# Optimization experiments

Measured on AMD Instinct MI355X. Metric: run time of the kernel, lower is better.

Reference implementation:

```python
import jax, jax.numpy as jnp
import numpy as np
from jax import lax

NUM_CLASSES = 21
MAX_OUT = 5          # max_output_size in tf.image.non_max_suppression
IOU_THR = 0.5        # NMS_IOU_THRESHOLD
CONF_THR = 0.5       # CONFIDENCE_THRESHOLD
NEG = -1e9           # stand-in for -inf score (suppressed / background)


def setup_inputs() -> dict:
    key = jax.random.key(0)
    k1, k2, k3 = jax.random.split(key, 3)
    B, N, C = 128, 8732, NUM_CLASSES
    logits = jax.random.normal(k1, (B, N, 4 + C), dtype=jnp.float32)
    # default boxes in corner format [ymin, xmin, ymax, xmax], valid geometry
    ctr = jax.random.uniform(k2, (N, 2), dtype=jnp.float32)                 # cy, cx
    sz = jax.random.uniform(k3, (N, 2), dtype=jnp.float32, minval=0.05, maxval=0.3)  # h, w
    default_boxes = jnp.clip(
        jnp.concatenate([ctr - sz / 2, ctr + sz / 2], axis=-1), 0.0, 1.0)
    return {"logits": logits, "default_boxes": default_boxes}


def _decode(loc, db):
    # db: [N,4] corners -> center/size (matches get_offset's tf.stack)
    cy = (db[:, 2] + db[:, 0]) / 2
    cx = (db[:, 3] + db[:, 1]) / 2
    h = db[:, 2] - db[:, 0]
    w = db[:, 3] - db[:, 1]
    # loc: [B,N,4] = (dy, dx, dh, dw)
    ncy = loc[..., 0] * h + cy
    ncx = loc[..., 1] * w + cx
    nh = jnp.exp(loc[..., 2]) * h
    nw = jnp.exp(loc[..., 3]) * w
    boxes = jnp.stack(
        [ncy - nh / 2, ncx - nw / 2, ncy + nh / 2, ncx + nw / 2], axis=-1)
    return jnp.clip(boxes, 0.0, 1.0)


def _iou_one_vs_all(box, boxes):
    # box [4], boxes [N,4], corner format
    tl = jnp.maximum(box[:2], boxes[:, :2])
    br = jnp.minimum(box[2:], boxes[:, 2:])
    wh = jnp.maximum(br - tl, 0.0)
    inter = wh[:, 0] * wh[:, 1]
    a1 = (box[2] - box[0]) * (box[3] - box[1])
    a2 = (boxes[:, 2] - boxes[:, 0]) * (boxes[:, 3] - boxes[:, 1])
    return inter / (a1 + a2 - inter + 1e-12)


def _nms_single(boxes, scores, classes_f):
    # boxes [N,4], scores [N] (background already set to NEG), classes_f [N] float
    def step(s, _):
        i = jnp.argmax(s)
        sc = s[i]
        b = boxes[i]
        valid = sc > CONF_THR  # score_threshold in tf NMS
        iou = _iou_one_vs_all(b, boxes)
        s = jnp.where(iou > IOU_THR, NEG, s)  # suppresses i too (IoU=1)
        return s, (b, classes_f[i], sc, valid)

    _, (bs, cs, ss, vs) = lax.scan(step, scores, None, length=MAX_OUT)
    # pad invalid slots with zeros (TF returns variable-length; we use fixed 5 + zero pad)
    bs = jnp.where(vs[:, None], bs, 0.0)
    cs = jnp.where(vs, cs, 0.0)
    ss = jnp.where(vs, ss, 0.0)
    return bs, cs[:, None], ss[:, None]  # [5,4], [5,1], [5,1]


def reference(logits, default_boxes):
    boxes = _decode(logits[..., :4], default_boxes)          # [B,N,4]
    probs = jax.nn.softmax(logits[..., 4:], axis=-1)         # [B,N,C]
    scores = jnp.max(probs, axis=-1)                          # [B,N]
    classes = jnp.argmax(probs, axis=-1)                      # [B,N] int
    # boolean_mask(classes != 0) expressed as score = -inf for background
    scores_eff = jnp.where(classes != 0, scores, NEG)
    det_b, det_c, det_s = jax.vmap(_nms_single)(
        boxes, scores_eff, classes.astype(jnp.float32))
    # pack detection_boxes / detection_classes / detection_scores -> [B,5,6]
    return jnp.concatenate([det_b, det_c, det_s], axis=-1)
```

## Files before the change

### kernel.cpp

```cpp
#include <hip/hip_runtime.h>

#define NEG (-1e9f)
constexpr int NCLS   = 21;
constexpr int NBOX   = 8732;
constexpr int MAXOUT = 5;
constexpr int CAP    = NBOX;
constexpr float IOU_THR  = 0.5f;
constexpr float CONF_THR = 0.5f;

__device__ __forceinline__ void process_box(
        const float* __restrict__ v,
        int idx,
        const float4* __restrict__ dbox4,
        float4* __restrict__ cand,
        int* __restrict__ cnt) {
    const int n = idx % NBOX;
    const int b = idx / NBOX;

    float4 db = dbox4[n];
    float cy = (db.z + db.x) * 0.5f;
    float cx = (db.w + db.y) * 0.5f;
    float h  = db.z - db.x;
    float w  = db.w - db.y;
    float ncy = v[0] * h + cy;
    float ncx = v[1] * w + cx;
    float nh  = expf(v[2]) * h;
    float nw  = expf(v[3]) * w;
    float y1 = fminf(fmaxf(ncy - nh * 0.5f, 0.f), 1.f);
    float x1 = fminf(fmaxf(ncx - nw * 0.5f, 0.f), 1.f);
    float y2 = fminf(fmaxf(ncy + nh * 0.5f, 0.f), 1.f);
    float x2 = fminf(fmaxf(ncx + nw * 0.5f, 0.f), 1.f);

    float m = v[4];
    int am = 0;
#pragma unroll
    for (int j = 1; j < NCLS; j++) {
        float x = v[4 + j];
        if (x > m) { m = x; am = j; }
    }
    float sum = 0.f;
#pragma unroll
    for (int j = 0; j < NCLS; j++) sum += expf(v[4 + j] - m);
    float score = 1.0f / sum;

    if (am != 0 && score > CONF_THR) {
        int p = atomicAdd(&cnt[b], 1);
        if (p < CAP) {
            float4* c = cand + ((long long)b * CAP + p) * 2;
            c[0] = make_float4(y1, x1, y2, x2);
            c[1] = make_float4(score, (float)am, (float)n, 0.f);
        }
    }
}

__global__ __launch_bounds__(128) void decode_kernel(
        const float* __restrict__ logits,
        const float4* __restrict__ dbox4,
        float4* __restrict__ cand,
        int* __restrict__ cnt,
        int BN) {
    const int g = (blockIdx.x * 128 + threadIdx.x) * 4;
    if (g >= BN) return;

    if (g + 3 < BN) {
        const float4* f4 = (const float4*)(logits + (long long)g * 25);
        float v[100];
#pragma unroll
        for (int k = 0; k < 25; k++) {
            float4 r = f4[k];
            v[4 * k + 0] = r.x; v[4 * k + 1] = r.y;
            v[4 * k + 2] = r.z; v[4 * k + 3] = r.w;
        }
#pragma unroll
        for (int j = 0; j < 4; j++)
            process_box(v + 25 * j, g + j, dbox4, cand, cnt);
    } else {
        for (int j = 0; j < 4 && g + j < BN; j++) {
            const float* L = logits + (long long)(g + j) * 25;
            float v[25];
#pragma unroll
            for (int k = 0; k < 25; k++) v[k] = L[k];
            process_box(v, g + j, dbox4, cand, cnt);
        }
    }
}

__global__ __launch_bounds__(64) void nms_kernel(
        const float4* __restrict__ cand,
        const int* __restrict__ cnt,
        float* __restrict__ out) {
    const int b    = blockIdx.x;
    const int lane = threadIdx.x;
    __shared__ float s_sc[CAP];
    __shared__ float s_id[CAP];

    const int M = min(cnt[b], CAP);
    const float4* cb = cand + (long long)b * CAP * 2;
    float* o = out + (long long)b * MAXOUT * 6;

    for (int i = lane; i < M; i += 64) {
        float4 mrec = cb[i * 2 + 1];
        s_sc[i] = mrec.x;
        s_id[i] = mrec.z;
    }

    int k = 0;
    for (; k < MAXOUT; k++) {
        float bv = -INFINITY, boid = 3.0e38f;
        int bi = -1;
        for (int i = lane; i < M; i += 64) {
            float v = s_sc[i], oid = s_id[i];
            if (v > bv || (v == bv && oid < boid)) { bv = v; boid = oid; bi = i; }
        }
        for (int mm = 32; mm >= 1; mm >>= 1) {
            float v2 = __shfl_xor(bv,   mm, 64);
            float o2 = __shfl_xor(boid, mm, 64);
            int   i2 = __shfl_xor(bi,   mm, 64);
            if (v2 > bv || (v2 == bv && o2 < boid)) { bv = v2; boid = o2; bi = i2; }
        }
        if (bi < 0 || !(bv > CONF_THR)) break;

        float4 sb = cb[bi * 2];
        if (lane == 0) {
            float4 mm2 = cb[bi * 2 + 1];
            o[k * 6 + 0] = sb.x; o[k * 6 + 1] = sb.y;
            o[k * 6 + 2] = sb.z; o[k * 6 + 3] = sb.w;
            o[k * 6 + 4] = mm2.y; o[k * 6 + 5] = bv;
        }

        float a1 = (sb.z - sb.x) * (sb.w - sb.y);
        for (int i = lane; i < M; i += 64) {
            float4 c = cb[i * 2];
            float tly = fmaxf(sb.x, c.x);
            float tlx = fmaxf(sb.y, c.y);
            float bry = fminf(sb.z, c.z);
            float brx = fminf(sb.w, c.w);
            float wh0 = fmaxf(bry - tly, 0.f);
            float wh1 = fmaxf(brx - tlx, 0.f);
            float inter = wh0 * wh1;
            float a2 = (c.z - c.x) * (c.w - c.y);
            float iou = inter / (a1 + a2 - inter + 1e-12f);
            if (iou > IOU_THR) s_sc[i] = NEG;
        }
    }
    for (int j = k * 6 + lane; j < MAXOUT * 6; j += 64) o[j] = 0.f;
}

extern "C" void kernel_launch(void* const* d_in, const int* in_sizes, int n_in,
                              void* d_out, int out_size, void* d_ws, size_t ws_size,
                              hipStream_t stream) {
    const float* logits = (const float*)d_in[0];
    const float4* dbox4 = (const float4*)d_in[1];
    float* out          = (float*)d_out;

    const int N  = in_sizes[1] / 4;
    const int B  = in_sizes[0] / (N * 25);
    const int BN = B * N;

    int* cnt = (int*)d_ws;
    float4* cand = (float4*)((char*)d_ws + (((size_t)B * sizeof(int) + 15) & ~(size_t)15));

    hipMemsetAsync(cnt, 0, (size_t)B * sizeof(int), stream);
    const int nthreads = (BN + 3) / 4;
    decode_kernel<<<(nthreads + 127) / 128, 128, 0, stream>>>(logits, dbox4, cand, cnt, BN);
    nms_kernel<<<B, 64, 0, stream>>>(cand, cnt, out);
}
```

Before: 190.2 us.

## Fuse decode and NMS into one kernel using a last-block-done counter

Merges the decode and NMS kernels into a single launch. Blocks are now grouped per batch image, and each block increments a per-batch done counter. The last finishing block for an image then runs the NMS for that image. This removes a kernel launch and lets NMS for early images overlap decode for others, but every block now reserves about 70KB of LDS for NMS scores, which may sharply limit occupancy during the bandwidth-bound decode phase.

Measured after the change: 374.1 us. +96.7%, slower.

```diff
diff --git a/kernel.cpp b/kernel.cpp
--- a/kernel.cpp
+++ b/kernel.cpp
@@ -8,15 +8,16 @@
 constexpr float IOU_THR  = 0.5f;
 constexpr float CONF_THR = 0.5f;
 
+constexpr int TPB             = 128;
+constexpr int BOXES_PER_BLOCK = TPB * 4;
+constexpr int BPB             = (NBOX + BOXES_PER_BLOCK - 1) / BOXES_PER_BLOCK;
+
 __device__ __forceinline__ void process_box(
         const float* __restrict__ v,
-        int idx,
+        int b, int n,
         const float4* __restrict__ dbox4,
         float4* __restrict__ cand,
         int* __restrict__ cnt) {
-    const int n = idx % NBOX;
-    const int b = idx / NBOX;
-
     float4 db = dbox4[n];
     float cy = (db.z + db.x) * 0.5f;
     float cx = (db.w + db.y) * 0.5f;
@@ -53,17 +54,24 @@
     }
 }
 
-__global__ __launch_bounds__(128) void decode_kernel(
+__global__ __launch_bounds__(TPB) void fused_kernel(
         const float* __restrict__ logits,
         const float4* __restrict__ dbox4,
         float4* __restrict__ cand,
         int* __restrict__ cnt,
-        int BN) {
-    const int g = (blockIdx.x * 128 + threadIdx.x) * 4;
-    if (g >= BN) return;
+        int* __restrict__ done,
+        float* __restrict__ out) {
+    const int b   = blockIdx.x / BPB;
+    const int blk = blockIdx.x % BPB;
+    const int n0  = blk * BOXES_PER_BLOCK + threadIdx.x * 4;
 
-    if (g + 3 < BN) {
-        const float4* f4 = (const float4*)(logits + (long long)g * 25);
+    __shared__ float s_sc[CAP];
+    __shared__ float s_id[CAP];
+    __shared__ int   s_last;
+
+    if (n0 < NBOX) {
+        const float4* f4 =
+            (const float4*)(logits + ((long long)b * NBOX + n0) * 25);
         float v[100];
 #pragma unroll
         for (int k = 0; k < 25; k++) {
@@ -73,27 +81,19 @@
         }
 #pragma unroll
         for (int j = 0; j < 4; j++)
-            process_box(v + 25 * j, g + j, dbox4, cand, cnt);
-    } else {
-        for (int j = 0; j < 4 && g + j < BN; j++) {
-            const float* L = logits + (long long)(g + j) * 25;
-            float v[25];
-#pragma unroll
-            for (int k = 0; k < 25; k++) v[k] = L[k];
-            process_box(v, g + j, dbox4, cand, cnt);
-        }
+            process_box(v + 25 * j, b, n0 + j, dbox4, cand, cnt);
     }
-}
 
-__global__ __launch_bounds__(64) void nms_kernel(
-        const float4* __restrict__ cand,
-        const int* __restrict__ cnt,
-        float* __restrict__ out) {
-    const int b    = blockIdx.x;
+    __threadfence();
+    __syncthreads();
+    if (threadIdx.x == 0)
+        s_last = (atomicAdd(&done[b], 1) == BPB - 1);
+    __syncthreads();
+    if (!s_last) return;
+    if (threadIdx.x >= 64) return;
+    __threadfence();
+
     const int lane = threadIdx.x;
-    __shared__ float s_sc[CAP];
-    __shared__ float s_id[CAP];
-
     const int M = min(cnt[b], CAP);
     const float4* cb = cand + (long long)b * CAP * 2;
     float* o = out + (long long)b * MAXOUT * 6;
@@ -153,15 +153,14 @@
     const float4* dbox4 = (const float4*)d_in[1];
     float* out          = (float*)d_out;
 
-    const int N  = in_sizes[1] / 4;
-    const int B  = in_sizes[0] / (N * 25);
-    const int BN = B * N;
+    const int N = in_sizes[1] / 4;
+    const int B = in_sizes[0] / (N * 25);
 
-    int* cnt = (int*)d_ws;
-    float4* cand = (float4*)((char*)d_ws + (((size_t)B * sizeof(int) + 15) & ~(size_t)15));
+    int* cnt  = (int*)d_ws;
+    int* done = cnt + B;
+    float4* cand = (float4*)((char*)d_ws +
+        ((2 * (size_t)B * sizeof(int) + 15) & ~(size_t)15));
 
-    hipMemsetAsync(cnt, 0, (size_t)B * sizeof(int), stream);
-    const int nthreads = (BN + 3) / 4;
-    decode_kernel<<<(nthreads + 127) / 128, 128, 0, stream>>>(logits, dbox4, cand, cnt, BN);
-    nms_kernel<<<B, 64, 0, stream>>>(cand, cnt, out);
+    hipMemsetAsync(d_ws, 0, 2 * (size_t)B * sizeof(int), stream);
+    fused_kernel<<<B * BPB, TPB, 0, stream>>>(logits, dbox4, cand, cnt, done, out);
 }
```
